# Performance work log

Hardware: AMD Instinct MI355X
Metric: run time of the kernel (lower is better)

The kernel has to match this reference:

```python
import jax, jax.numpy as jnp
import numpy as np

NEG_SLOPE = 0.2  # PyG GATConv default negative_slope
EPS = 1e-16      # PyG softmax denominator epsilon


def gat_conv(x, src, dst, W, b, att_src, att_dst, num_nodes):
    """PyG GATConv, heads=1, add_self_loops=True (self loops already in src/dst).
    x: [N, Fin]; src/dst: [E]; W: [Fin, Fout]; att_src/att_dst: [Fout]."""
    h = x @ W                                  # [N, Fout]
    a_src = h @ att_src                        # [N]
    a_dst = h @ att_dst                        # [N]
    e = jax.nn.leaky_relu(a_src[src] + a_dst[dst], NEG_SLOPE)  # [E]
    m = jax.ops.segment_max(e, dst, num_segments=num_nodes)    # softmax over edges grouped by dst
    ex = jnp.exp(e - m[dst])
    denom = jax.ops.segment_sum(ex, dst, num_segments=num_nodes)
    alpha = ex / (denom[dst] + EPS)            # [E]
    out = jax.ops.segment_sum(alpha[:, None] * h[src], dst, num_segments=num_nodes)
    return out + b


def global_attention(x, gate_w, gate_b):
    """PyG GlobalAttention with a single graph: softmax(gate_nn(x)) weighted sum."""
    gate = x @ gate_w + gate_b                 # [N, 1]
    attn = jax.nn.softmax(gate, axis=0)        # softmax over all nodes (one graph)
    return jnp.sum(attn * x, axis=0, keepdims=True)  # [1, F]


def setup_inputs() -> dict:
    key = jax.random.key(0)
    ks = jax.random.split(key, 12)
    N, E, D, H = 50000, 800000, 768, 256
    x = jax.random.normal(ks[0], (N, D), dtype=jnp.float32)
    edge_index = jax.random.randint(ks[1], (2, E), 0, N, dtype=jnp.int64)
    s = 1.0 / np.sqrt(D)
    W1 = jax.random.normal(ks[2], (D, H), dtype=jnp.float32) * s
    b1 = jnp.zeros((H,), dtype=jnp.float32)
    as1 = jax.random.normal(ks[3], (H,), dtype=jnp.float32) * (1.0 / np.sqrt(H))
    ad1 = jax.random.normal(ks[4], (H,), dtype=jnp.float32) * (1.0 / np.sqrt(H))
    s2 = 1.0 / np.sqrt(H)
    W2 = jax.random.normal(ks[5], (H, H), dtype=jnp.float32) * s2
    b2 = jnp.zeros((H,), dtype=jnp.float32)
    as2 = jax.random.normal(ks[6], (H,), dtype=jnp.float32) * s2
    ad2 = jax.random.normal(ks[7], (H,), dtype=jnp.float32) * s2
    gate_w = jax.random.normal(ks[8], (H, 1), dtype=jnp.float32) * s2
    gate_b = jnp.zeros((1,), dtype=jnp.float32)
    return {"x": x, "edge_index": edge_index, "W1": W1, "b1": b1, "as1": as1,
            "ad1": ad1, "W2": W2, "b2": b2, "as2": as2, "ad2": ad2,
            "gate_w": gate_w, "gate_b": gate_b}


def reference(x, edge_index, W1, b1, as1, ad1, W2, b2, as2, ad2, gate_w, gate_b):
    N = x.shape[0]
    loops = jnp.arange(N, dtype=edge_index.dtype)
    src = jnp.concatenate([edge_index[0], loops])  # add self loops (GATConv default)
    dst = jnp.concatenate([edge_index[1], loops])
    h = gat_conv(x, src, dst, W1, b1, as1, ad1, N)
    h = jax.nn.relu(h)
    h = gat_conv(h, src, dst, W2, b2, as2, ad2, N)
    h = jax.nn.relu(h)
    return global_attention(h, gate_w, gate_b)   # [1, 256]
```

## Files before the change

kernel.cpp:

```cpp
#include <hip/hip_runtime.h>

#define WAVE 64
#define LRELU(x) ((x) > 0.0f ? (x) : 0.2f * (x))
#define SB0 __builtin_amdgcn_sched_barrier(0)

typedef __attribute__((ext_vector_type(8))) short bf16x8;
typedef __attribute__((ext_vector_type(8))) unsigned short u16x8;
typedef __attribute__((ext_vector_type(4))) float f32x4;

__device__ __forceinline__ void gld16(const void* g, void* l) {
    __builtin_amdgcn_global_load_lds((const __attribute__((address_space(1))) unsigned int*)g,
                                     (__attribute__((address_space(3))) unsigned int*)l,
                                     16, 0, 0);
}

__device__ __forceinline__ unsigned short f2bf_hi(float f) {
    unsigned u = __builtin_bit_cast(unsigned, f);
    u += 0x7FFF + ((u >> 16) & 1);
    return (unsigned short)(u >> 16);
}

__device__ __forceinline__ void split8(f32x4 a, f32x4 b, bf16x8& hi, bf16x8& lo) {
    float f[8] = {a[0], a[1], a[2], a[3], b[0], b[1], b[2], b[3]};
#pragma unroll
    for (int e = 0; e < 8; e++) {
        unsigned u = __builtin_bit_cast(unsigned, f[e]);
        float hf = __builtin_bit_cast(float, u & 0xFFFF0000u);
        float fl = f[e] - hf;
        unsigned u2 = __builtin_bit_cast(unsigned, fl);
        unsigned t2 = u2 + 0x7FFF + ((u2 >> 16) & 1);
        hi[e] = (short)(u >> 16);
        lo[e] = (short)(t2 >> 16);
    }
}

__device__ __forceinline__ void split8t(f32x4 a, f32x4 b, bf16x8& hi, bf16x8& lo) {
    float f[8] = {a[0], a[1], a[2], a[3], b[0], b[1], b[2], b[3]};
#pragma unroll
    for (int e = 0; e < 8; e++) {
        unsigned u = __builtin_bit_cast(unsigned, f[e]);
        float hf = __builtin_bit_cast(float, u & 0xFFFF0000u);
        float fl = f[e] - hf;
        unsigned u2 = __builtin_bit_cast(unsigned, fl);
        hi[e] = (short)(u >> 16);
        lo[e] = (short)(u2 >> 16);
    }
}

__global__ __launch_bounds__(256) void k_gemm_f32A(const float* __restrict__ A,
                                                   const unsigned short* __restrict__ Bh,
                                                   unsigned short* __restrict__ Cb,
                                                   float* __restrict__ asrc,
                                                   float* __restrict__ adst,
                                                   const float* __restrict__ att_s,
                                                   const float* __restrict__ att_d,
                                                   int M, int K) {
    __shared__ char smem[49152];
    char* bA = smem;
    char* bB = smem + 32768;

    const int tid = threadIdx.x, lane = tid & 63, w = tid >> 6;
    const int m16 = lane & 15, q = lane >> 4;
    const int row0 = blockIdx.x * 128, col0 = blockIdx.y * 128;
    const int NT = K >> 5;

    f32x4 acc[4][4];
#pragma unroll
    for (int i = 0; i < 4; i++)
#pragma unroll
        for (int j = 0; j < 4; j++) acc[i][j] = (f32x4){0.f, 0.f, 0.f, 0.f};

    const float* apt[4];
    const int jA0 = w * 4;
#pragma unroll
    for (int jj = 0; jj < 4; jj++) {
        int j = jA0 + jj;
        int r = j * 8 + (lane >> 3);
        int grow = row0 + r;
        if (grow > M - 1) grow = M - 1;
        int s = (lane & 7) ^ ((lane >> 3) & 7);
        apt[jj] = A + (size_t)grow * K + s * 4;
    }
    const unsigned short* bpt[2];
    const int jB0 = w * 2;
#pragma unroll
    for (int jj = 0; jj < 2; jj++) {
        int j = jB0 + jj;
        int r = j * 16 + (lane >> 2);
        int s = (lane & 3) ^ ((lane >> 3) & 3);
        bpt[jj] = Bh + (size_t)(col0 + r) * K + s * 8;
    }

    auto stageA = [&](int t, int buf) {
#pragma unroll
        for (int jj = 0; jj < 4; jj++)
            gld16(apt[jj] + (size_t)t * 32, bA + buf * 16384 + (jA0 + jj) * 1024);
    };
    auto stageB = [&](int t, int buf) {
#pragma unroll
        for (int jj = 0; jj < 2; jj++)
            gld16(bpt[jj] + (size_t)t * 32, bB + buf * 8192 + (jB0 + jj) * 1024);
    };

    stageB(0, 0); SB0;
    stageA(0, 0); SB0;
    asm volatile("s_waitcnt vmcnt(0)" ::: "memory");
    __builtin_amdgcn_s_barrier();

    for (int t = 0; t < NT; ++t) {
        if (t + 1 < NT) {
            stageB(t + 1, (t + 1) & 1);
            stageA(t + 1, (t + 1) & 1);
        }
        SB0;

        const char* A_ = bA + (t & 1) * 16384;
        const char* B_ = bB + (t & 1) * 8192;
        bf16x8 bh[4];
#pragma unroll
        for (int nt = 0; nt < 4; nt++) {
            int r = (w & 1) * 64 + nt * 16 + m16;
            int p = q ^ ((r >> 1) & 3);
            bh[nt] = *(const bf16x8*)(B_ + r * 64 + p * 16);
        }
#pragma unroll
        for (int mt = 0; mt < 4; mt++) {
            int r = (w >> 1) * 64 + mt * 16 + m16;
            int p0 = (2 * q) ^ (r & 7);
            int p1 = (2 * q + 1) ^ (r & 7);
            f32x4 a0 = *(const f32x4*)(A_ + r * 128 + p0 * 16);
            f32x4 a1 = *(const f32x4*)(A_ + r * 128 + p1 * 16);
            bf16x8 ah, al;
            split8t(a0, a1, ah, al);
#pragma unroll
            for (int nt = 0; nt < 4; nt++) {
                acc[mt][nt] = __builtin_amdgcn_mfma_f32_16x16x32_bf16(ah, bh[nt], acc[mt][nt], 0, 0, 0);
                acc[mt][nt] = __builtin_amdgcn_mfma_f32_16x16x32_bf16(al, bh[nt], acc[mt][nt], 0, 0, 0);
            }
        }
        SB0;
        asm volatile("s_waitcnt vmcnt(0)" ::: "memory");
        __builtin_amdgcn_s_barrier();
    }

    const int rbase = row0 + (w >> 1) * 64;
    const int cbase = col0 + (w & 1) * 64;
#pragma unroll
    for (int mt = 0; mt < 4; mt++)
#pragma unroll
        for (int r = 0; r < 4; r++) {
            int row = rbase + mt * 16 + q * 4 + r;
            if (row < M) {
#pragma unroll
                for (int nt = 0; nt < 4; nt++)
                    Cb[(size_t)row * 256 + cbase + nt * 16 + m16] = f2bf_hi(acc[mt][nt][r]);
            }
        }
    float as_v[4], ad_v[4];
#pragma unroll
    for (int nt = 0; nt < 4; nt++) {
        as_v[nt] = att_s[cbase + nt * 16 + m16];
        ad_v[nt] = att_d[cbase + nt * 16 + m16];
    }
#pragma unroll
    for (int mt = 0; mt < 4; mt++)
#pragma unroll
        for (int r = 0; r < 4; r++) {
            float s = 0.f, d = 0.f;
#pragma unroll
            for (int nt = 0; nt < 4; nt++) {
                float v = acc[mt][nt][r];
                s = fmaf(v, as_v[nt], s);
                d = fmaf(v, ad_v[nt], d);
            }
#pragma unroll
            for (int off = 1; off < 16; off <<= 1) {
                s += __shfl_xor(s, off);
                d += __shfl_xor(d, off);
            }
            int row = rbase + mt * 16 + q * 4 + r;
            if (m16 == 0 && row < M) {
                atomicAdd(&asrc[row], s);
                atomicAdd(&adst[row], d);
            }
        }
}

__global__ __launch_bounds__(256) void k_gemm_bf16A(const unsigned short* __restrict__ Ah,
                                                    const unsigned short* __restrict__ Al,
                                                    const unsigned short* __restrict__ Bh,
                                                    unsigned short* __restrict__ Cb,
                                                    float* __restrict__ asrc,
                                                    float* __restrict__ adst,
                                                    const float* __restrict__ att_s,
                                                    const float* __restrict__ att_d,
                                                    int M, int K) {
    __shared__ char smem[49152];
    char* bAh = smem;
    char* bAl = smem + 16384;
    char* bB  = smem + 32768;

    const int tid = threadIdx.x, lane = tid & 63, w = tid >> 6;
    const int m16 = lane & 15, q = lane >> 4;
    const int row0 = blockIdx.x * 128, col0 = blockIdx.y * 128;
    const int NT = K >> 5;

    f32x4 acc[4][4];
#pragma unroll
    for (int i = 0; i < 4; i++)
#pragma unroll
        for (int j = 0; j < 4; j++) acc[i][j] = (f32x4){0.f, 0.f, 0.f, 0.f};

    const unsigned short* ahpt[2];
    const unsigned short* alpt[2];
    const unsigned short* bpt[2];
    const int j0 = w * 2;
#pragma unroll
    for (int jj = 0; jj < 2; jj++) {
        int j = j0 + jj;
        int r = j * 16 + (lane >> 2);
        int s = (lane & 3) ^ ((lane >> 3) & 3);
        ahpt[jj] = Ah + (size_t)(row0 + r) * K + s * 8;
        alpt[jj] = Al + (size_t)(row0 + r) * K + s * 8;
        bpt[jj]  = Bh + (size_t)(col0 + r) * K + s * 8;
    }

    auto stageAll = [&](int t, int buf) {
#pragma unroll
        for (int jj = 0; jj < 2; jj++)
            gld16(bpt[jj] + (size_t)t * 32, bB + buf * 8192 + (j0 + jj) * 1024);
#pragma unroll
        for (int jj = 0; jj < 2; jj++)
            gld16(ahpt[jj] + (size_t)t * 32, bAh + buf * 8192 + (j0 + jj) * 1024);
#pragma unroll
        for (int jj = 0; jj < 2; jj++)
            gld16(alpt[jj] + (size_t)t * 32, bAl + buf * 8192 + (j0 + jj) * 1024);
    };

    stageAll(0, 0); SB0;
    asm volatile("s_waitcnt vmcnt(0)" ::: "memory");
    __builtin_amdgcn_s_barrier();

    for (int t = 0; t < NT; ++t) {
        if (t + 1 < NT) stageAll(t + 1, (t + 1) & 1);
        SB0;

        const char* Ah_ = bAh + (t & 1) * 8192;
        const char* Al_ = bAl + (t & 1) * 8192;
        const char* B_  = bB  + (t & 1) * 8192;
        bf16x8 bh[4];
#pragma unroll
        for (int nt = 0; nt < 4; nt++) {
            int r = (w & 1) * 64 + nt * 16 + m16;
            int p = q ^ ((r >> 1) & 3);
            bh[nt] = *(const bf16x8*)(B_ + r * 64 + p * 16);
        }
#pragma unroll
        for (int mt = 0; mt < 4; mt++) {
            int r = (w >> 1) * 64 + mt * 16 + m16;
            int p = q ^ ((r >> 1) & 3);
            bf16x8 ah = *(const bf16x8*)(Ah_ + r * 64 + p * 16);
            bf16x8 al = *(const bf16x8*)(Al_ + r * 64 + p * 16);
#pragma unroll
            for (int nt = 0; nt < 4; nt++) {
                acc[mt][nt] = __builtin_amdgcn_mfma_f32_16x16x32_bf16(ah, bh[nt], acc[mt][nt], 0, 0, 0);
                acc[mt][nt] = __builtin_amdgcn_mfma_f32_16x16x32_bf16(al, bh[nt], acc[mt][nt], 0, 0, 0);
            }
        }
        SB0;
        asm volatile("s_waitcnt vmcnt(0)" ::: "memory");
        __builtin_amdgcn_s_barrier();
    }

    const int rbase = row0 + (w >> 1) * 64;
    const int cbase = col0 + (w & 1) * 64;
#pragma unroll
    for (int mt = 0; mt < 4; mt++)
#pragma unroll
        for (int r = 0; r < 4; r++) {
            int row = rbase + mt * 16 + q * 4 + r;
            if (row < M) {
#pragma unroll
                for (int nt = 0; nt < 4; nt++)
                    Cb[(size_t)row * 256 + cbase + nt * 16 + m16] = f2bf_hi(acc[mt][nt][r]);
            }
        }
    float as_v[4], ad_v[4];
#pragma unroll
    for (int nt = 0; nt < 4; nt++) {
        as_v[nt] = att_s[cbase + nt * 16 + m16];
        ad_v[nt] = att_d[cbase + nt * 16 + m16];
    }
#pragma unroll
    for (int mt = 0; mt < 4; mt++)
#pragma unroll
        for (int r = 0; r < 4; r++) {
            float s = 0.f, d = 0.f;
#pragma unroll
            for (int nt = 0; nt < 4; nt++) {
                float v = acc[mt][nt][r];
                s = fmaf(v, as_v[nt], s);
                d = fmaf(v, ad_v[nt], d);
            }
#pragma unroll
            for (int off = 1; off < 16; off <<= 1) {
                s += __shfl_xor(s, off);
                d += __shfl_xor(d, off);
            }
            int row = rbase + mt * 16 + q * 4 + r;
            if (m16 == 0 && row < M) {
                atomicAdd(&asrc[row], s);
                atomicAdd(&adst[row], d);
            }
        }
}

__global__ __launch_bounds__(256) void k_convB(const float* __restrict__ W,
                                               unsigned short* __restrict__ BThi, int K) {
    int idx = blockIdx.x * 256 + threadIdx.x;
    int k = idx >> 8, n = idx & 255;
    if (k >= K) return;
    BThi[(size_t)n * K + k] = f2bf_hi(W[(size_t)k * 256 + n]);
}

__global__ __launch_bounds__(256) void k_degree(const int* __restrict__ dst,
                                                int* __restrict__ counts, int E) {
    int e = blockIdx.x * 256 + threadIdx.x;
    if (e < E) atomicAdd(&counts[dst[e]], 1);
}

__global__ __launch_bounds__(256) void k_part(const int* __restrict__ counts,
                                              int* __restrict__ psum, int N) {
    __shared__ int red[256];
    int tid = threadIdx.x;
    int i = blockIdx.x * 256 + tid;
    red[tid] = (i < N) ? counts[i] : 0;
    __syncthreads();
    for (int off = 128; off; off >>= 1) {
        if (tid < off) red[tid] += red[tid + off];
        __syncthreads();
    }
    if (tid == 0) psum[blockIdx.x] = red[0];
}

__global__ __launch_bounds__(256) void k_scan_part(int* __restrict__ psum, int nb,
                                                   int* __restrict__ total_out) {
    __shared__ int s[256];
    int tid = threadIdx.x;
    int v = (tid < nb) ? psum[tid] : 0;
    s[tid] = v;
    __syncthreads();
    for (int off = 1; off < 256; off <<= 1) {
        int t = (tid >= off) ? s[tid - off] : 0;
        __syncthreads();
        s[tid] += t;
        __syncthreads();
    }
    if (tid < nb) psum[tid] = s[tid] - v;
    if (tid == 255) *total_out = s[255];
}

__global__ __launch_bounds__(256) void k_rowptr(const int* __restrict__ counts,
                                                const int* __restrict__ psum,
                                                int* __restrict__ rowptr,
                                                int* __restrict__ cursor, int N) {
    __shared__ int s[256];
    int tid = threadIdx.x;
    int i = blockIdx.x * 256 + tid;
    int v = (i < N) ? counts[i] : 0;
    s[tid] = v;
    __syncthreads();
    for (int off = 1; off < 256; off <<= 1) {
        int t = (tid >= off) ? s[tid - off] : 0;
        __syncthreads();
        s[tid] += t;
        __syncthreads();
    }
    if (i < N) {
        int excl = psum[blockIdx.x] + s[tid] - v;
        rowptr[i] = excl;
        cursor[i] = excl;
    }
}

__global__ __launch_bounds__(256) void k_scatter(const int* __restrict__ src,
                                                 const int* __restrict__ dst,
                                                 int* __restrict__ cursor,
                                                 int* __restrict__ col, int E) {
    int e = blockIdx.x * 256 + threadIdx.x;
    if (e < E) {
        int p = atomicAdd(&cursor[dst[e]], 1);
        col[p] = src[e];
    }
}

__global__ __launch_bounds__(256) void k_edge(const unsigned short* __restrict__ hb,
                                              const float* __restrict__ asrc,
                                              const float* __restrict__ adst,
                                              const float* __restrict__ gmaxv,
                                              const int* __restrict__ rowptr,
                                              const int* __restrict__ col,
                                              const float* __restrict__ bias,
                                              float* __restrict__ outf,
                                              unsigned short* __restrict__ outh,
                                              unsigned short* __restrict__ outl,
                                              const float* __restrict__ gw,
                                              const float* __restrict__ gb,
                                              float* __restrict__ gatep, int N) {
    int hw = threadIdx.x >> 5;
    int l  = threadIdx.x & 31;
    int node = blockIdx.x * 8 + hw;
    if (node >= N) return;
    int j = rowptr[node], end = rowptr[node + 1];
    float ad = adst[node];
    float m = LRELU(gmaxv[0] + ad);

    float a[8];
    float wself = __expf(LRELU(asrc[node] + ad) - m);
    u16x8 hv = *(const u16x8*)&hb[(size_t)node * 256 + l * 8];
#pragma unroll
    for (int e = 0; e < 8; e++)
        a[e] = wself * __builtin_bit_cast(float, (unsigned)hv[e] << 16);
    float denom = wself;

    for (; j + 4 <= end; j += 4) {
        int s0 = col[j], s1 = col[j + 1], s2 = col[j + 2], s3 = col[j + 3];
        float w0 = __expf(LRELU(asrc[s0] + ad) - m);
        float w1 = __expf(LRELU(asrc[s1] + ad) - m);
        float w2 = __expf(LRELU(asrc[s2] + ad) - m);
        float w3 = __expf(LRELU(asrc[s3] + ad) - m);
        denom += w0 + w1 + w2 + w3;
        u16x8 h0 = *(const u16x8*)&hb[(size_t)s0 * 256 + l * 8];
        u16x8 h1 = *(const u16x8*)&hb[(size_t)s1 * 256 + l * 8];
        u16x8 h2 = *(const u16x8*)&hb[(size_t)s2 * 256 + l * 8];
        u16x8 h3 = *(const u16x8*)&hb[(size_t)s3 * 256 + l * 8];
#pragma unroll
        for (int e = 0; e < 8; e++) {
            float f0 = __builtin_bit_cast(float, (unsigned)h0[e] << 16);
            float f1 = __builtin_bit_cast(float, (unsigned)h1[e] << 16);
            float f2 = __builtin_bit_cast(float, (unsigned)h2[e] << 16);
            float f3 = __builtin_bit_cast(float, (unsigned)h3[e] << 16);
            a[e] = fmaf(w0, f0, fmaf(w1, f1, fmaf(w2, f2, fmaf(w3, f3, a[e]))));
        }
    }
    for (; j < end; j++) {
        int s = col[j];
        float wgt = __expf(LRELU(asrc[s] + ad) - m);
        denom += wgt;
        u16x8 hx = *(const u16x8*)&hb[(size_t)s * 256 + l * 8];
#pragma unroll
        for (int e = 0; e < 8; e++)
            a[e] = fmaf(wgt, __builtin_bit_cast(float, (unsigned)hx[e] << 16), a[e]);
    }
    float inv = 1.0f / (denom + 1e-16f);
#pragma unroll
    for (int e = 0; e < 8; e++) a[e] *= inv;

    float o[8];
    {
        float4 bv0 = *(const float4*)&bias[l * 8];
        float4 bv1 = *(const float4*)&bias[l * 8 + 4];
        float bb[8] = {bv0.x, bv0.y, bv0.z, bv0.w, bv1.x, bv1.y, bv1.z, bv1.w};
#pragma unroll
        for (int e = 0; e < 8; e++) o[e] = fmaxf(a[e] + bb[e], 0.0f);
    }
    if (outf) {
        float4 o0 = make_float4(o[0], o[1], o[2], o[3]);
        float4 o1 = make_float4(o[4], o[5], o[6], o[7]);
        *(float4*)&outf[(size_t)node * 256 + l * 8]     = o0;
        *(float4*)&outf[(size_t)node * 256 + l * 8 + 4] = o1;
    }
    if (outh) {
        u16x8 ph, pl;
#pragma unroll
        for (int e = 0; e < 8; e++) {
            unsigned u = __builtin_bit_cast(unsigned, o[e]);
            float hf = __builtin_bit_cast(float, u & 0xFFFF0000u);
            float fl = o[e] - hf;
            unsigned u2 = __builtin_bit_cast(unsigned, fl);
            unsigned t2 = u2 + 0x7FFF + ((u2 >> 16) & 1);
            ph[e] = (unsigned short)(u >> 16);
            pl[e] = (unsigned short)(t2 >> 16);
        }
        *(u16x8*)&outh[(size_t)node * 256 + l * 8] = ph;
        *(u16x8*)&outl[(size_t)node * 256 + l * 8] = pl;
    }
    if (gatep) {
        float s = 0.f;
#pragma unroll
        for (int e = 0; e < 8; e++) s = fmaf(o[e], gw[l * 8 + e], s);
#pragma unroll
        for (int off = 16; off; off >>= 1) s += __shfl_xor(s, off);
        if (l == 0) gatep[node] = s + gb[0];
    }
}

__global__ __launch_bounds__(256) void k_pmax(const float* __restrict__ v, int N,
                                              float* __restrict__ pmax) {
    __shared__ float red[256];
    int tid = threadIdx.x;
    float m = -3.0e38f;
    for (int i = blockIdx.x * 256 + tid; i < N; i += gridDim.x * 256) m = fmaxf(m, v[i]);
    red[tid] = m;
    __syncthreads();
    for (int off = 128; off; off >>= 1) {
        if (tid < off) red[tid] = fmaxf(red[tid], red[tid + off]);
        __syncthreads();
    }
    if (tid == 0) pmax[blockIdx.x] = red[0];
}

__global__ __launch_bounds__(64) void k_fold(const float* __restrict__ p,
                                             float* __restrict__ o) {
    int lane = threadIdx.x;
    float m = p[lane];
#pragma unroll
    for (int off = 32; off; off >>= 1) m = fmaxf(m, __shfl_xor(m, off));
    if (lane == 0) o[0] = m;
}

__global__ __launch_bounds__(256) void k_gmid(const float* __restrict__ pmax, int nb,
                                              float* __restrict__ scal,
                                              float* __restrict__ gout) {
    __shared__ float red[256];
    int tid = threadIdx.x;
    red[tid] = (tid < nb) ? pmax[tid] : -3.0e38f;
    __syncthreads();
    for (int off = 128; off; off >>= 1) {
        if (tid < off) red[tid] = fmaxf(red[tid], red[tid + off]);
        __syncthreads();
    }
    if (tid == 0) { scal[0] = red[0]; scal[1] = 0.0f; }
    gout[tid] = 0.0f;
}

__global__ __launch_bounds__(256) void k_gout(const float* __restrict__ h,
                                              const float* __restrict__ gate,
                                              float* __restrict__ scal_rw,
                                              float* __restrict__ gout, int N) {
    int f = threadIdx.x;
    float gmax = scal_rw[0];
    float acc = 0.0f, sumw = 0.0f;
    for (int i = blockIdx.x; i < N; i += gridDim.x) {
        float w = __expf(gate[i] - gmax);
        acc = fmaf(w, h[(size_t)i * 256 + f], acc);
        sumw += w;
    }
    atomicAdd(&gout[f], acc);
    if (f == 0) atomicAdd(&scal_rw[1], sumw);
}

__global__ __launch_bounds__(256) void k_final(const float* __restrict__ gout,
                                               const float* __restrict__ scal,
                                               float* __restrict__ out) {
    int f = threadIdx.x;
    out[f] = gout[f] / scal[1];
}

extern "C" void kernel_launch(void* const* d_in, const int* in_sizes, int n_in,
                              void* d_out, int out_size, void* d_ws, size_t ws_size,
                              hipStream_t stream) {
    const float* x   = (const float*)d_in[0];
    const int*   ei  = (const int*)d_in[1];
    const float* W1  = (const float*)d_in[2];
    const float* b1  = (const float*)d_in[3];
    const float* as1 = (const float*)d_in[4];
    const float* ad1 = (const float*)d_in[5];
    const float* W2  = (const float*)d_in[6];
    const float* b2  = (const float*)d_in[7];
    const float* as2 = (const float*)d_in[8];
    const float* ad2 = (const float*)d_in[9];
    const float* gw  = (const float*)d_in[10];
    const float* gb  = (const float*)d_in[11];
    float* out = (float*)d_out;

    const int N = in_sizes[0] / 768;
    const int E = in_sizes[1] / 2;
    const int Mpad = (N + 127) & ~127;
    const int* srcA = ei;
    const int* dstA = ei + E;

    char* w = (char*)d_ws;
    auto alloc = [&](size_t bytes) -> void* {
        void* p = (void*)w;
        w += (bytes + 255) & ~(size_t)255;
        return p;
    };
    unsigned short* bufHb = (unsigned short*)alloc((size_t)N * 256 * 2);
    unsigned short* X2h = (unsigned short*)alloc((size_t)Mpad * 256 * 2);
    unsigned short* X2l = (unsigned short*)alloc((size_t)Mpad * 256 * 2);
    float* bufX = (float*)X2h;
    float* asrc   = (float*)alloc((size_t)N * 4);
    float* adst   = (float*)alloc((size_t)N * 4);
    float* gate   = (float*)alloc((size_t)N * 4);
    int*   counts = (int*)alloc((size_t)N * 4);
    int*   rowptr = (int*)alloc((size_t)(N + 1) * 4);
    int*   cursor = (int*)alloc((size_t)N * 4);
    int*   colbuf = (int*)alloc((size_t)E * 4);
    int*   psum   = (int*)alloc(256 * 4);
    float* pmax   = (float*)alloc(256 * 4);
    float* gmaxv  = (float*)alloc(4 * 4);
    float* scal   = (float*)alloc(8 * 4);
    float* gout   = (float*)alloc(256 * 4);
    unsigned short* BT1 = (unsigned short*)alloc((size_t)256 * 768 * 2);
    unsigned short* BT2 = (unsigned short*)alloc((size_t)256 * 256 * 2);

    const int eb  = (E + 255) / 256;
    const int nb8 = (N + 7) / 8;
    const int nb  = (N + 255) / 256;
    const dim3 gg(Mpad / 128, 2);

    k_convB<<<768, 256, 0, stream>>>(W1, BT1, 768);
    k_convB<<<256, 256, 0, stream>>>(W2, BT2, 256);

    (void)hipMemsetAsync(counts, 0, (size_t)N * 4, stream);
    k_degree<<<eb, 256, 0, stream>>>(dstA, counts, E);
    k_part<<<nb, 256, 0, stream>>>(counts, psum, N);
    k_scan_part<<<1, 256, 0, stream>>>(psum, nb, rowptr + N);
    k_rowptr<<<nb, 256, 0, stream>>>(counts, psum, rowptr, cursor, N);
    k_scatter<<<eb, 256, 0, stream>>>(srcA, dstA, cursor, colbuf, E);

    (void)hipMemsetAsync(asrc, 0, (size_t)N * 4, stream);
    (void)hipMemsetAsync(adst, 0, (size_t)N * 4, stream);
    k_gemm_f32A<<<gg, 256, 0, stream>>>(x, BT1, bufHb, asrc, adst, as1, ad1, N, 768);
    k_pmax<<<64, 256, 0, stream>>>(asrc, N, pmax);
    k_fold<<<1, 64, 0, stream>>>(pmax, gmaxv);
    k_edge<<<nb8, 256, 0, stream>>>(bufHb, asrc, adst, gmaxv, rowptr, colbuf, b1,
                                    nullptr, X2h, X2l, nullptr, nullptr, nullptr, N);

    (void)hipMemsetAsync(asrc, 0, (size_t)N * 4, stream);
    (void)hipMemsetAsync(adst, 0, (size_t)N * 4, stream);
    k_gemm_bf16A<<<gg, 256, 0, stream>>>(X2h, X2l, BT2, bufHb, asrc, adst, as2, ad2, N, 256);
    k_pmax<<<64, 256, 0, stream>>>(asrc, N, pmax);
    k_fold<<<1, 64, 0, stream>>>(pmax, gmaxv);
    k_edge<<<nb8, 256, 0, stream>>>(bufHb, asrc, adst, gmaxv, rowptr, colbuf, b2,
                                    bufX, nullptr, nullptr, gw, gb, gate, N);

    k_pmax<<<64, 256, 0, stream>>>(gate, N, pmax);
    k_gmid<<<1, 256, 0, stream>>>(pmax, 64, scal, gout);
    k_gout<<<256, 256, 0, stream>>>(bufX, gate, scal, gout, N);
    k_final<<<1, 256, 0, stream>>>(gout, scal, out);
}
```

Measured before the change: 599.4 us.

## Load B fragments directly to registers and triple-buffer A tiles in LDS

Both GEMM kernels stop staging the bf16 weight tile through LDS. Each wave now loads its B fragments straight from global memory into double-buffered registers one K-step ahead. The A tiles move to a three-deep LDS ring prefetched two steps ahead, with partial vmcnt waits so loads overlap the MFMA work. The intent is to hide global latency better and cut LDS traffic and barrier stalls, at the cost of more VGPRs and uncoalesced per-lane B reads. The loop is also unrolled by two, which assumes NT is even.

```diff
diff --git a/kernel.cpp b/kernel.cpp
--- a/kernel.cpp
+++ b/kernel.cpp
@@ -57,7 +57,6 @@
                                                    int M, int K) {
     __shared__ char smem[49152];
     char* bA = smem;
-    char* bB = smem + 32768;
 
     const int tid = threadIdx.x, lane = tid & 63, w = tid >> 6;
     const int m16 = lane & 15, q = lane >> 4;
@@ -81,48 +80,34 @@
         int s = (lane & 7) ^ ((lane >> 3) & 7);
         apt[jj] = A + (size_t)grow * K + s * 4;
     }
-    const unsigned short* bpt[2];
-    const int jB0 = w * 2;
-#pragma unroll
-    for (int jj = 0; jj < 2; jj++) {
-        int j = jB0 + jj;
-        int r = j * 16 + (lane >> 2);
-        int s = (lane & 3) ^ ((lane >> 3) & 3);
-        bpt[jj] = Bh + (size_t)(col0 + r) * K + s * 8;
-    }
-
     auto stageA = [&](int t, int buf) {
 #pragma unroll
         for (int jj = 0; jj < 4; jj++)
             gld16(apt[jj] + (size_t)t * 32, bA + buf * 16384 + (jA0 + jj) * 1024);
     };
-    auto stageB = [&](int t, int buf) {
-#pragma unroll
-        for (int jj = 0; jj < 2; jj++)
-            gld16(bpt[jj] + (size_t)t * 32, bB + buf * 8192 + (jB0 + jj) * 1024);
-    };
-
-    stageB(0, 0); SB0;
+
+    const unsigned short* bbase = Bh + (size_t)(col0 + (w & 1) * 64 + m16) * K + q * 8;
+    bf16x8 bh0[4], bh1[4];
+
+#pragma unroll
+    for (int nt = 0; nt < 4; nt++)
+        bh0[nt] = *(const bf16x8*)(bbase + (size_t)nt * 16 * K);
+    SB0;
     stageA(0, 0); SB0;
-    asm volatile("s_waitcnt vmcnt(0)" ::: "memory");
+    stageA(1, 1); SB0;
+    asm volatile("s_waitcnt vmcnt(4)" ::: "memory");
     __builtin_amdgcn_s_barrier();
 
-    for (int t = 0; t < NT; ++t) {
+    auto body = [&](int t, bf16x8 (&cur)[4], bf16x8 (&nxt)[4]) {
         if (t + 1 < NT) {
-            stageB(t + 1, (t + 1) & 1);
-            stageA(t + 1, (t + 1) & 1);
+#pragma unroll
+            for (int nt = 0; nt < 4; nt++)
+                nxt[nt] = *(const bf16x8*)(bbase + (size_t)nt * 16 * K + (size_t)(t + 1) * 32);
         }
         SB0;
-
-        const char* A_ = bA + (t & 1) * 16384;
-        const char* B_ = bB + (t & 1) * 8192;
-        bf16x8 bh[4];
-#pragma unroll
-        for (int nt = 0; nt < 4; nt++) {
-            int r = (w & 1) * 64 + nt * 16 + m16;
-            int p = q ^ ((r >> 1) & 3);
-            bh[nt] = *(const bf16x8*)(B_ + r * 64 + p * 16);
-        }
+        if (t + 2 < NT) stageA(t + 2, (t + 2) % 3);
+        SB0;
+        const char* A_ = bA + (t % 3) * 16384;
 #pragma unroll
         for (int mt = 0; mt < 4; mt++) {
             int r = (w >> 1) * 64 + mt * 16 + m16;
@@ -134,13 +119,19 @@
             split8t(a0, a1, ah, al);
 #pragma unroll
             for (int nt = 0; nt < 4; nt++) {
-                acc[mt][nt] = __builtin_amdgcn_mfma_f32_16x16x32_bf16(ah, bh[nt], acc[mt][nt], 0, 0, 0);
-                acc[mt][nt] = __builtin_amdgcn_mfma_f32_16x16x32_bf16(al, bh[nt], acc[mt][nt], 0, 0, 0);
+                acc[mt][nt] = __builtin_amdgcn_mfma_f32_16x16x32_bf16(ah, cur[nt], acc[mt][nt], 0, 0, 0);
+                acc[mt][nt] = __builtin_amdgcn_mfma_f32_16x16x32_bf16(al, cur[nt], acc[mt][nt], 0, 0, 0);
             }
         }
         SB0;
-        asm volatile("s_waitcnt vmcnt(0)" ::: "memory");
+        if (t + 2 < NT)      asm volatile("s_waitcnt vmcnt(8)" ::: "memory");
+        else if (t + 1 < NT) asm volatile("s_waitcnt vmcnt(4)" ::: "memory");
+        else                 asm volatile("s_waitcnt vmcnt(0)" ::: "memory");
         __builtin_amdgcn_s_barrier();
+    };
+    for (int t = 0; t < NT; t += 2) {
+        body(t, bh0, bh1);
+        body(t + 1, bh1, bh0);
     }
 
     const int rbase = row0 + (w >> 1) * 64;
@@ -196,9 +187,7 @@
                                                     const float* __restrict__ att_d,
                                                     int M, int K) {
     __shared__ char smem[49152];
-    char* bAh = smem;
-    char* bAl = smem + 16384;
-    char* bB  = smem + 32768;
+    char* bA = smem;
 
     const int tid = threadIdx.x, lane = tid & 63, w = tid >> 6;
     const int m16 = lane & 15, q = lane >> 4;
@@ -213,7 +202,6 @@
 
     const unsigned short* ahpt[2];
     const unsigned short* alpt[2];
-    const unsigned short* bpt[2];
     const int j0 = w * 2;
 #pragma unroll
     for (int jj = 0; jj < 2; jj++) {
@@ -222,39 +210,39 @@
         int s = (lane & 3) ^ ((lane >> 3) & 3);
         ahpt[jj] = Ah + (size_t)(row0 + r) * K + s * 8;
         alpt[jj] = Al + (size_t)(row0 + r) * K + s * 8;
-        bpt[jj]  = Bh + (size_t)(col0 + r) * K + s * 8;
-    }
-
-    auto stageAll = [&](int t, int buf) {
+    }
+    auto stageA = [&](int t, int buf) {
 #pragma unroll
         for (int jj = 0; jj < 2; jj++)
-            gld16(bpt[jj] + (size_t)t * 32, bB + buf * 8192 + (j0 + jj) * 1024);
+            gld16(ahpt[jj] + (size_t)t * 32, bA + buf * 16384 + (j0 + jj) * 1024);
 #pragma unroll
         for (int jj = 0; jj < 2; jj++)
-            gld16(ahpt[jj] + (size_t)t * 32, bAh + buf * 8192 + (j0 + jj) * 1024);
-#pragma unroll
-        for (int jj = 0; jj < 2; jj++)
-            gld16(alpt[jj] + (size_t)t * 32, bAl + buf * 8192 + (j0 + jj) * 1024);
+            gld16(alpt[jj] + (size_t)t * 32, bA + buf * 16384 + 8192 + (j0 + jj) * 1024);
     };
 
-    stageAll(0, 0); SB0;
-    asm volatile("s_waitcnt vmcnt(0)" ::: "memory");
+    const unsigned short* bbase = Bh + (size_t)(col0 + (w & 1) * 64 + m16) * K + q * 8;
+    bf16x8 bh0[4], bh1[4];
+
+#pragma unroll
+    for (int nt = 0; nt < 4; nt++)
+        bh0[nt] = *(const bf16x8*)(bbase + (size_t)nt * 16 * K);
+    SB0;
+    stageA(0, 0); SB0;
+    stageA(1, 1); SB0;
+    asm volatile("s_waitcnt vmcnt(4)" ::: "memory");
     __builtin_amdgcn_s_barrier();
 
-    for (int t = 0; t < NT; ++t) {
-        if (t + 1 < NT) stageAll(t + 1, (t + 1) & 1);
+    auto body = [&](int t, bf16x8 (&cur)[4], bf16x8 (&nxt)[4]) {
+        if (t + 1 < NT) {
+#pragma unroll
+            for (int nt = 0; nt < 4; nt++)
+                nxt[nt] = *(const bf16x8*)(bbase + (size_t)nt * 16 * K + (size_t)(t + 1) * 32);
+        }
         SB0;
-
-        const char* Ah_ = bAh + (t & 1) * 8192;
-        const char* Al_ = bAl + (t & 1) * 8192;
-        const char* B_  = bB  + (t & 1) * 8192;
-        bf16x8 bh[4];
-#pragma unroll
-        for (int nt = 0; nt < 4; nt++) {
-            int r = (w & 1) * 64 + nt * 16 + m16;
-            int p = q ^ ((r >> 1) & 3);
-            bh[nt] = *(const bf16x8*)(B_ + r * 64 + p * 16);
-        }
+        if (t + 2 < NT) stageA(t + 2, (t + 2) % 3);
+        SB0;
+        const char* Ah_ = bA + (t % 3) * 16384;
+        const char* Al_ = Ah_ + 8192;
 #pragma unroll
         for (int mt = 0; mt < 4; mt++) {
             int r = (w >> 1) * 64 + mt * 16 + m16;
@@ -263,13 +251,19 @@
             bf16x8 al = *(const bf16x8*)(Al_ + r * 64 + p * 16);
 #pragma unroll
             for (int nt = 0; nt < 4; nt++) {
-                acc[mt][nt] = __builtin_amdgcn_mfma_f32_16x16x32_bf16(ah, bh[nt], acc[mt][nt], 0, 0, 0);
-                acc[mt][nt] = __builtin_amdgcn_mfma_f32_16x16x32_bf16(al, bh[nt], acc[mt][nt], 0, 0, 0);
+                acc[mt][nt] = __builtin_amdgcn_mfma_f32_16x16x32_bf16(ah, cur[nt], acc[mt][nt], 0, 0, 0);
+                acc[mt][nt] = __builtin_amdgcn_mfma_f32_16x16x32_bf16(al, cur[nt], acc[mt][nt], 0, 0, 0);
             }
         }
         SB0;
-        asm volatile("s_waitcnt vmcnt(0)" ::: "memory");
+        if (t + 2 < NT)      asm volatile("s_waitcnt vmcnt(8)" ::: "memory");
+        else if (t + 1 < NT) asm volatile("s_waitcnt vmcnt(4)" ::: "memory");
+        else                 asm volatile("s_waitcnt vmcnt(0)" ::: "memory");
         __builtin_amdgcn_s_barrier();
+    };
+    for (int t = 0; t < NT; t += 2) {
+        body(t, bh0, bh1);
+        body(t + 1, bh1, bh0);
     }
 
     const int rbase = row0 + (w >> 1) * 64;
```

Result: slower. 624.4 us (+4.2%).
